# Performance work log

Measured on AMD Instinct MI355X. Metric: run time of the kernel, lower is better.

The kernel has to match this reference:

```python
import jax, jax.numpy as jnp
import numpy as np

# SLAYER neuron params (from network.yaml defaults)
THETA = 10.0      # spike threshold
TAU_SR = 10.0     # synaptic (PSP) time constant
TAU_REF = 1.0     # refractory time constant
SCALE_REF = 2.0   # refractory strength (in units of theta)
TAU_RHO = 1.0     # surrogate-gradient width
SCALE_RHO = 1.0   # surrogate-gradient scale
TS = 1.0          # simulation timestep


@jax.custom_vjp
def spike_heaviside(u):
    # SLAYER spike generation: hard threshold in forward
    return (u >= THETA).astype(u.dtype)

def _spk_fwd(u):
    return spike_heaviside(u), u

def _spk_bwd(u, g):
    # SLAYER surrogate: rho(u) = (scaleRho/tauRho) * exp(-|u - theta| / tauRho)
    surr = (SCALE_RHO / TAU_RHO) * jnp.exp(-jnp.abs(u - THETA) / TAU_RHO)
    return (g * surr,)

spike_heaviside.defvjp(_spk_fwd, _spk_bwd)


def psp(x):
    """Temporal post-synaptic-potential filter (exponential synapse kernel).
    x: (B, T, F) -> (B, T, F);  p[t] = decay * p[t-1] + x[t]."""
    decay = jnp.exp(jnp.asarray(-TS / TAU_SR, x.dtype))
    def step(p, xt):
        p = decay * p + xt
        return p, p
    p0 = jnp.zeros((x.shape[0], x.shape[2]), x.dtype)
    _, ps = jax.lax.scan(step, p0, jnp.swapaxes(x, 0, 1))  # scan over T
    return jnp.swapaxes(ps, 0, 1)


def spike(u):
    """Thresholded spike generation with refractory feedback.
    u: (B, T, F) membrane input; refractory state subtracts 2*theta after a spike
    and decays with tauRef (SLAYER refractory response)."""
    decay_ref = jnp.exp(jnp.asarray(-TS / TAU_REF, u.dtype))
    def step(r, ut):
        v = ut + r
        s = spike_heaviside(v)
        r = decay_ref * (r - SCALE_REF * THETA * s)
        return r, s
    r0 = jnp.zeros((u.shape[0], u.shape[2]), u.dtype)
    _, ss = jax.lax.scan(step, r0, jnp.swapaxes(u, 0, 1))  # scan over T
    return jnp.swapaxes(ss, 0, 1)


def setup_inputs() -> dict:
    key = jax.random.key(0)
    k1, k2, k3 = jax.random.split(key, 3)
    B, T, F_IN, F_H, F_OUT = 64, 500, 1250, 512, 2
    x = (jax.random.uniform(k1, (B, T, F_IN)) < 0.1).astype(jnp.float32)
    W1 = jax.random.normal(k2, (F_H, F_IN), jnp.float32) * 0.05
    W2 = jax.random.normal(k3, (F_OUT, F_H), jnp.float32) * 0.05
    return {"x": x, "W1": W1, "W2": W2}


def reference(x, W1, W2):
    # layer 1: dense projection per timestep -> PSP filter -> spike
    s1 = spike(psp(jnp.einsum('btf,hf->bth', x, W1)))   # (B, T, 512)
    # layer 2
    out = spike(psp(jnp.einsum('bth,oh->bto', s1, W2))) # (B, T, 2)
    return out
```

## Files before the change

kernel.cpp:

```cpp
#include <hip/hip_runtime.h>
#include <hip/hip_bf16.h>
#include <cstdint>
#include <cstddef>

#define B_N   64
#define T_N   500
#define K_IN  1250
#define KP    1280
#define N_H   512
#define M_N   32000

#define BM 128
#define BN 256
#define BK 32
#define NT (KP / BK)
#define XROWB (KP / 8)

typedef __attribute__((ext_vector_type(8))) short bf16x8;
typedef __attribute__((ext_vector_type(4))) float f32x4;

#define DECAY_SR  0.9048374180359595732f
#define DECAY_REF 0.3678794411714423216f
#define THETA 10.0f

__device__ __forceinline__ unsigned short f2bf(float f) {
  __hip_bfloat16 h = __float2bfloat16(f);
  return *reinterpret_cast<unsigned short*>(&h);
}
__device__ __forceinline__ float bf2f(unsigned short s) {
  union { uint32_t u; float f; } v; v.u = ((uint32_t)s) << 16; return v.f;
}

__global__ __launch_bounds__(256) void xpack_kernel(const float* __restrict__ X,
                                                    unsigned long long* __restrict__ Xb64) {
  int gw   = (blockIdx.x * 256 + threadIdx.x) >> 6;
  int lane = threadIdx.x & 63;
  const float* xr = X + (size_t)gw * K_IN;
  unsigned long long* out = Xb64 + (size_t)gw * (XROWB / 8);
  #pragma unroll
  for (int wd = 0; wd < 20; ++wd) {
    int k = wd * 64 + lane;
    float v = (k < K_IN) ? xr[k] : 0.f;
    unsigned long long m = __ballot(v > 0.5f);
    if (lane == 0) out[wd] = m;
  }
}

__global__ __launch_bounds__(256) void w1cvt_kernel(const float* __restrict__ W1,
                                                    short* __restrict__ W1b) {
  int k = blockIdx.x * 256 + threadIdx.x;
  int n = blockIdx.y;
  float v = (k < K_IN) ? W1[(size_t)n * K_IN + k] : 0.f;
  W1b[(size_t)n * KP + k] = (short)f2bf(v);
}

__global__ __launch_bounds__(256) void gemm1_kernel(const unsigned char* __restrict__ Xb,
                                                    const short* __restrict__ W1b,
                                                    unsigned short* __restrict__ U1) {
  __shared__ short Bs[2][BN * BK];
  __shared__ short LUT[256 * 8];
  const int tid  = threadIdx.x;
  const int bn   = blockIdx.x * BN;
  const int bm   = blockIdx.y * BM;
  const int w    = tid >> 6;
  const int lane = tid & 63;
  const int wr   = w >> 1;
  const int wc   = w & 1;
  const int lrow = lane & 15;
  const int lgrp = lane >> 4;
  const int lsw  = lgrp ^ ((lrow >> 1) & 3);

  {
    int b = tid;
    uint32_t w0 = ((b & 1)  ? 0x3F80u : 0u) | ((b & 2)  ? 0x3F800000u : 0u);
    uint32_t w1 = ((b & 4)  ? 0x3F80u : 0u) | ((b & 8)  ? 0x3F800000u : 0u);
    uint32_t w2 = ((b & 16) ? 0x3F80u : 0u) | ((b & 32) ? 0x3F800000u : 0u);
    uint32_t w3 = ((b & 64) ? 0x3F80u : 0u) | ((b & 128)? 0x3F800000u : 0u);
    uint4 q; q.x = w0; q.y = w1; q.z = w2; q.w = w3;
    *(uint4*)&LUT[b * 8] = q;
  }

  f32x4 acc[4][8];
  #pragma unroll
  for (int i = 0; i < 4; ++i)
    #pragma unroll
    for (int j = 0; j < 8; ++j)
      acc[i][j] = (f32x4){0.f, 0.f, 0.f, 0.f};

  const int brow16 = lane >> 2;
  const int bslp   = lane & 3;
  const unsigned char* xb0 = Xb + (size_t)(bm + wr * 64 + lrow) * XROWB + lgrp;

  auto stageB = [&](int buf, int k0) {
    #pragma unroll
    for (int c = 0; c < 4; ++c) {
      int ch = w * 4 + c;
      int nl = ch * 16 + brow16;
      int ss = bslp ^ ((nl >> 1) & 3);
      const short* src = W1b + (size_t)(bn + nl) * KP + k0 + ss * 8;
      __builtin_amdgcn_global_load_lds(
          (const __attribute__((address_space(1))) void*)src,
          (__attribute__((address_space(3))) void*)&Bs[buf][ch * 16 * BK], 16, 0, 0);
    }
  };

  stageB(0, 0);
  unsigned char c0 = xb0[0];
  unsigned char c1 = xb0[16 * XROWB];
  unsigned char c2 = xb0[32 * XROWB];
  unsigned char c3 = xb0[48 * XROWB];
  __syncthreads();

  int pb = 0;
  for (int t = 0; t < NT; ++t) {
    unsigned char n0 = c0, n1 = c1, n2 = c2, n3 = c3;
    if (t + 1 < NT) {
      stageB(pb ^ 1, (t + 1) * BK);
      const unsigned char* xbn = xb0 + (t + 1) * 4;
      n0 = xbn[0];
      n1 = xbn[16 * XROWB];
      n2 = xbn[32 * XROWB];
      n3 = xbn[48 * XROWB];
    }
    bf16x8 af[4];
    af[0] = *(const bf16x8*)&LUT[(int)c0 * 8];
    af[1] = *(const bf16x8*)&LUT[(int)c1 * 8];
    af[2] = *(const bf16x8*)&LUT[(int)c2 * 8];
    af[3] = *(const bf16x8*)&LUT[(int)c3 * 8];
    bf16x8 bv[8];
    #pragma unroll
    for (int j = 0; j < 8; ++j) {
      int r = wc * 128 + j * 16 + lrow;
      bv[j] = *(const bf16x8*)&Bs[pb][r * BK + lsw * 8];
    }
    #pragma unroll
    for (int i = 0; i < 4; ++i)
      #pragma unroll
      for (int j = 0; j < 8; ++j)
        acc[i][j] = __builtin_amdgcn_mfma_f32_16x16x32_bf16(af[i], bv[j], acc[i][j], 0, 0, 0);
    __syncthreads();
    pb ^= 1;
    c0 = n0; c1 = n1; c2 = n2; c3 = n3;
  }

  #pragma unroll
  for (int i = 0; i < 4; ++i) {
    int row0 = bm + wr * 64 + i * 16 + lgrp * 4;
    #pragma unroll
    for (int j = 0; j < 8; ++j) {
      int col = bn + wc * 128 + j * 16 + lrow;
      #pragma unroll
      for (int r = 0; r < 4; ++r)
        U1[(size_t)(row0 + r) * N_H + col] = f2bf(acc[i][j][r]);
    }
  }
}

__global__ __launch_bounds__(128) void scan1_kernel(const unsigned short* __restrict__ U1,
                                                    unsigned long long* __restrict__ S1m) {
  int idx  = blockIdx.x * 128 + threadIdx.x;
  int b    = idx >> 9, h = idx & 511;
  int lane = threadIdx.x & 63;
  const unsigned short* u = U1 + (size_t)b * T_N * N_H + h;
  unsigned long long* mout = S1m + (size_t)b * T_N * 8 + (h >> 6);
  float p = 0.f, r = 0.f;
  float bufA[10], bufB[10];

  auto load = [&](float* buf, int t0) {
    #pragma unroll
    for (int j = 0; j < 10; ++j) buf[j] = bf2f(u[(size_t)(t0 + j) * N_H]);
  };
  auto proc = [&](const float* buf, int t0) {
    #pragma unroll
    for (int j = 0; j < 10; ++j) {
      p = DECAY_SR * p + buf[j];
      float v = p + r;
      bool sp = (v >= THETA);
      r = DECAY_REF * (r - (sp ? 2.f * THETA : 0.f));
      unsigned long long bal = __ballot(sp);
      if (lane == 0) mout[(size_t)(t0 + j) * 8] = bal;
    }
  };

  load(bufA, 0);
  for (int g = 0; g < 25; ++g) {
    int ta = g * 20, tb = ta + 10;
    load(bufB, tb);
    proc(bufA, ta);
    if (g < 24) load(bufA, tb + 10);
    proc(bufB, tb);
  }
}

__global__ __launch_bounds__(256) void gemm2_kernel(const unsigned char* __restrict__ S1b,
                                                    const float* __restrict__ W2,
                                                    float* __restrict__ U2) {
  int m    = blockIdx.x * 4 + (threadIdx.x >> 6);
  int lane = threadIdx.x & 63;
  unsigned int byte = S1b[(size_t)m * 64 + lane];
  float a0 = 0.f, a1 = 0.f;
  #pragma unroll
  for (int j = 0; j < 8; ++j) {
    int h = lane * 8 + j;
    float sel = ((byte >> j) & 1u) ? 1.f : 0.f;
    a0 += sel * W2[h];
    a1 += sel * W2[N_H + h];
  }
  #pragma unroll
  for (int off = 32; off >= 1; off >>= 1) {
    a0 += __shfl_down(a0, off);
    a1 += __shfl_down(a1, off);
  }
  if (lane == 0) {
    U2[(size_t)m * 2]     = a0;
    U2[(size_t)m * 2 + 1] = a1;
  }
}

__global__ __launch_bounds__(128) void scan2_kernel(const float* __restrict__ U2,
                                                    float* __restrict__ OUT) {
  __shared__ float lu[T_N * 2];
  __shared__ float ls[T_N * 2];
  int b = blockIdx.x;
  const float* src = U2 + (size_t)b * T_N * 2;
  for (int i = threadIdx.x; i < T_N * 2; i += 128) lu[i] = src[i];
  __syncthreads();
  if (threadIdx.x < 2) {
    int o = threadIdx.x;
    float p = 0.f, r = 0.f;
    for (int t = 0; t < T_N; ++t) {
      p = DECAY_SR * p + lu[t * 2 + o];
      float v = p + r;
      float sp = (v >= THETA) ? 1.f : 0.f;
      r = DECAY_REF * (r - 2.f * THETA * sp);
      ls[t * 2 + o] = sp;
    }
  }
  __syncthreads();
  float* dst = OUT + (size_t)b * T_N * 2;
  for (int i = threadIdx.x; i < T_N * 2; i += 128) dst[i] = ls[i];
}

extern "C" void kernel_launch(void* const* d_in, const int* in_sizes, int n_in,
                              void* d_out, int out_size, void* d_ws, size_t ws_size,
                              hipStream_t stream) {
  const float* X  = (const float*)d_in[0];
  const float* W1 = (const float*)d_in[1];
  const float* W2 = (const float*)d_in[2];
  float* OUT = (float*)d_out;

  char* ws = (char*)d_ws;
  short*              W1b = (short*)ws;
  unsigned short*     U1  = (unsigned short*)(ws + 1310720);
  unsigned long long* S1m = (unsigned long long*)(ws + 34078720);
  float*              U2  = (float*)(ws + 36126720);
  unsigned long long* Xb  = (unsigned long long*)(ws + 36382720);

  xpack_kernel<<<dim3(M_N / 4), 256, 0, stream>>>(X, Xb);
  w1cvt_kernel<<<dim3(KP / 256, N_H), 256, 0, stream>>>(W1, (short*)W1b);
  gemm1_kernel<<<dim3(N_H / BN, M_N / BM), 256, 0, stream>>>((const unsigned char*)Xb, W1b, U1);
  scan1_kernel<<<dim3((B_N * N_H) / 128), 128, 0, stream>>>(U1, S1m);
  gemm2_kernel<<<dim3(M_N / 4), 256, 0, stream>>>((const unsigned char*)S1m, W2, U2);
  scan2_kernel<<<dim3(B_N), 128, 0, stream>>>(U2, OUT);
}
```

Before: 362.9 us.

## Stage packed A bits via async LDS loads with 3-deep prefetch; widen scan1 buffers

GEMM1 now loads the packed input-spike bytes into LDS with global_load_lds alongside the W1 tiles, replacing per-thread global byte loads. Prefetch runs two tiles ahead using explicit vmcnt waits and split barriers, instead of one tile ahead. The bf16 A fragments are expanded from bits in registers rather than through a shared-memory lookup table. The scan1 kernel raises its register buffers from 10 to 25 timesteps to keep more loads in flight, at the cost of extra register pressure.

```diff
diff --git a/kernel.cpp b/kernel.cpp
--- a/kernel.cpp
+++ b/kernel.cpp
@@ -58,7 +58,7 @@
                                                     const short* __restrict__ W1b,
                                                     unsigned short* __restrict__ U1) {
   __shared__ short Bs[2][BN * BK];
-  __shared__ short LUT[256 * 8];
+  __shared__ unsigned int Ab[2][BM];
   const int tid  = threadIdx.x;
   const int bn   = blockIdx.x * BN;
   const int bm   = blockIdx.y * BM;
@@ -70,16 +70,6 @@
   const int lgrp = lane >> 4;
   const int lsw  = lgrp ^ ((lrow >> 1) & 3);
 
-  {
-    int b = tid;
-    uint32_t w0 = ((b & 1)  ? 0x3F80u : 0u) | ((b & 2)  ? 0x3F800000u : 0u);
-    uint32_t w1 = ((b & 4)  ? 0x3F80u : 0u) | ((b & 8)  ? 0x3F800000u : 0u);
-    uint32_t w2 = ((b & 16) ? 0x3F80u : 0u) | ((b & 32) ? 0x3F800000u : 0u);
-    uint32_t w3 = ((b & 64) ? 0x3F80u : 0u) | ((b & 128)? 0x3F800000u : 0u);
-    uint4 q; q.x = w0; q.y = w1; q.z = w2; q.w = w3;
-    *(uint4*)&LUT[b * 8] = q;
-  }
-
   f32x4 acc[4][8];
   #pragma unroll
   for (int i = 0; i < 4; ++i)
@@ -89,9 +79,9 @@
 
   const int brow16 = lane >> 2;
   const int bslp   = lane & 3;
-  const unsigned char* xb0 = Xb + (size_t)(bm + wr * 64 + lrow) * XROWB + lgrp;
-
-  auto stageB = [&](int buf, int k0) {
+
+  auto stage = [&](int buf, int t) {
+    int k0 = t * BK;
     #pragma unroll
     for (int c = 0; c < 4; ++c) {
       int ch = w * 4 + c;
@@ -102,45 +92,53 @@
           (const __attribute__((address_space(1))) void*)src,
           (__attribute__((address_space(3))) void*)&Bs[buf][ch * 16 * BK], 16, 0, 0);
     }
+    if (lane < 32) {
+      const unsigned char* srcA = Xb + (size_t)(bm + w * 32 + lane) * XROWB + t * 4;
+      __builtin_amdgcn_global_load_lds(
+          (const __attribute__((address_space(1))) void*)srcA,
+          (__attribute__((address_space(3))) void*)&Ab[buf][w * 32], 4, 0, 0);
+    }
   };
 
-  stageB(0, 0);
-  unsigned char c0 = xb0[0];
-  unsigned char c1 = xb0[16 * XROWB];
-  unsigned char c2 = xb0[32 * XROWB];
-  unsigned char c3 = xb0[48 * XROWB];
+  stage(0, 0);
+  stage(1, 1);
   __syncthreads();
 
-  int pb = 0;
   for (int t = 0; t < NT; ++t) {
-    unsigned char n0 = c0, n1 = c1, n2 = c2, n3 = c3;
-    if (t + 1 < NT) {
-      stageB(pb ^ 1, (t + 1) * BK);
-      const unsigned char* xbn = xb0 + (t + 1) * 4;
-      n0 = xbn[0];
-      n1 = xbn[16 * XROWB];
-      n2 = xbn[32 * XROWB];
-      n3 = xbn[48 * XROWB];
-    }
-    bf16x8 af[4];
-    af[0] = *(const bf16x8*)&LUT[(int)c0 * 8];
-    af[1] = *(const bf16x8*)&LUT[(int)c1 * 8];
-    af[2] = *(const bf16x8*)&LUT[(int)c2 * 8];
-    af[3] = *(const bf16x8*)&LUT[(int)c3 * 8];
+    const int pb = t & 1;
+    unsigned int aw[4];
+    #pragma unroll
+    for (int i = 0; i < 4; ++i)
+      aw[i] = Ab[pb][wr * 64 + i * 16 + lrow];
     bf16x8 bv[8];
     #pragma unroll
     for (int j = 0; j < 8; ++j) {
       int r = wc * 128 + j * 16 + lrow;
       bv[j] = *(const bf16x8*)&Bs[pb][r * BK + lsw * 8];
+    }
+    bf16x8 af[4];
+    #pragma unroll
+    for (int i = 0; i < 4; ++i) {
+      unsigned int b = (aw[i] >> (lgrp * 8)) & 0xFFu;
+      #pragma unroll
+      for (int e = 0; e < 8; ++e)
+        af[i][e] = (short)(((b >> e) & 1u) * 0x3F80u);
     }
     #pragma unroll
     for (int i = 0; i < 4; ++i)
       #pragma unroll
       for (int j = 0; j < 8; ++j)
         acc[i][j] = __builtin_amdgcn_mfma_f32_16x16x32_bf16(af[i], bv[j], acc[i][j], 0, 0, 0);
-    __syncthreads();
-    pb ^= 1;
-    c0 = n0; c1 = n1; c2 = n2; c3 = n3;
+
+    asm volatile("s_waitcnt lgkmcnt(0)" ::: "memory");
+    __builtin_amdgcn_s_barrier();
+    if (t + 2 < NT) {
+      stage(pb, t + 2);
+      asm volatile("s_waitcnt vmcnt(5)" ::: "memory");
+    } else {
+      asm volatile("s_waitcnt vmcnt(0)" ::: "memory");
+    }
+    __builtin_amdgcn_s_barrier();
   }
 
   #pragma unroll
@@ -164,15 +162,15 @@
   const unsigned short* u = U1 + (size_t)b * T_N * N_H + h;
   unsigned long long* mout = S1m + (size_t)b * T_N * 8 + (h >> 6);
   float p = 0.f, r = 0.f;
-  float bufA[10], bufB[10];
+  float bufA[25], bufB[25];
 
   auto load = [&](float* buf, int t0) {
     #pragma unroll
-    for (int j = 0; j < 10; ++j) buf[j] = bf2f(u[(size_t)(t0 + j) * N_H]);
+    for (int j = 0; j < 25; ++j) buf[j] = bf2f(u[(size_t)(t0 + j) * N_H]);
   };
   auto proc = [&](const float* buf, int t0) {
     #pragma unroll
-    for (int j = 0; j < 10; ++j) {
+    for (int j = 0; j < 25; ++j) {
       p = DECAY_SR * p + buf[j];
       float v = p + r;
       bool sp = (v >= THETA);
@@ -183,11 +181,11 @@
   };
 
   load(bufA, 0);
-  for (int g = 0; g < 25; ++g) {
-    int ta = g * 20, tb = ta + 10;
+  for (int g = 0; g < 10; ++g) {
+    int ta = g * 50, tb = ta + 25;
     load(bufB, tb);
     proc(bufA, ta);
-    if (g < 24) load(bufA, tb + 10);
+    if (g < 9) load(bufA, tb + 25);
     proc(bufB, tb);
   }
 }
@@ -257,7 +255,7 @@
   unsigned long long* Xb  = (unsigned long long*)(ws + 36382720);
 
   xpack_kernel<<<dim3(M_N / 4), 256, 0, stream>>>(X, Xb);
-  w1cvt_kernel<<<dim3(KP / 256, N_H), 256, 0, stream>>>(W1, (short*)W1b);
+  w1cvt_kernel<<<dim3(KP / 256, N_H), 256, 0, stream>>>(W1, W1b);
   gemm1_kernel<<<dim3(N_H / BN, M_N / BM), 256, 0, stream>>>((const unsigned char*)Xb, W1b, U1);
   scan1_kernel<<<dim3((B_N * N_H) / 128), 128, 0, stream>>>(U1, S1m);
   gemm2_kernel<<<dim3(M_N / 4), 256, 0, stream>>>((const unsigned char*)S1m, W2, U2);
```

New measurement: 387.8 us. 6.8% more time.
